# Kernel tuning notes

Hardware: AMD Instinct MI355X
Metric: run time of the kernel (lower is better)

The kernel has to match this reference:

```python
import jax, jax.numpy as jnp
import numpy as np

B, N, P, D, NH, DFFN = 4, 1024, 128, 512, 8, 2048
DH = D // NH  # 64


def setup_inputs() -> dict:
    key = jax.random.key(0)
    ks = jax.random.split(key, 64)
    i = [0]
    def rn(shape, s=1.0):
        k = ks[i[0]]; i[0] += 1
        return jax.random.normal(k, shape, jnp.float32) * s
    w = 0.05  # weight init scale
    inp = {
        "H": rn((B, N, D)),
        "V": rn((B, N, 3, D)),
        "D_batch": rn((B, N, N)),
        "rbf_bias": rn((B, 1, N, N)),  # rbf_feat_batch[layer_idx]
        "prompt_feature": rn((B * P, D)),
        # self-attn params
        "Wq": rn((4 * D, D), w), "bq": jnp.zeros((4 * D,), jnp.float32),
        "Wk": rn((4 * D, D), w), "bk": jnp.zeros((4 * D,), jnp.float32),
        "Wv": rn((D, D), w), "bv": jnp.zeros((D,), jnp.float32),
        "Wvv": rn((D, D), w),
        "Wo": rn((D, D), w), "bo": jnp.zeros((D,), jnp.float32),
        "Wvo": rn((D, D), w),
        "ln1_g": jnp.ones((D,), jnp.float32), "ln1_b": jnp.zeros((D,), jnp.float32),
        # cross-attn params (nn.MultiheadAttention packed in_proj + out_proj, then scaler_o)
        "ca_in_w": rn((3 * D, D), w), "ca_in_b": jnp.zeros((3 * D,), jnp.float32),
        "ca_out_w": rn((D, D), w), "ca_out_b": jnp.zeros((D,), jnp.float32),
        "ca_so_w": rn((D, D), w), "ca_so_b": jnp.zeros((D,), jnp.float32),
        "ln2_g": jnp.ones((D,), jnp.float32), "ln2_b": jnp.zeros((D,), jnp.float32),
        # GVP-FFN params
        "ffn_lv": rn((2 * D, D), w),
        "ffn_w1": rn((DFFN, 2 * D), w), "ffn_b1": jnp.zeros((DFFN,), jnp.float32),
        "ffn_w2": rn((2 * D, DFFN), w), "ffn_b2": jnp.zeros((2 * D,), jnp.float32),
        "ln3_g": jnp.ones((D,), jnp.float32), "ln3_b": jnp.zeros((D,), jnp.float32),
        # key-validity mask [B,N]
        "H_mask": jax.random.randint(ks[60], (B, N), 0, 2).astype(jnp.int32),
    }
    return inp


def _ln(x, g, b):
    m = x.mean(-1, keepdims=True)
    v = ((x - m) ** 2).mean(-1, keepdims=True)
    return (x - m) / jnp.sqrt(v + 1e-5) * g + b


def _ept_layer(H, V, D_batch, rbf_bias, prompt_feature,
               Wq, bq, Wk, bk, Wv, bv, Wvv, Wo, bo, Wvo, ln1_g, ln1_b,
               ca_in_w, ca_in_b, ca_out_w, ca_out_b, ca_so_w, ca_so_b, ln2_g, ln2_b,
               ffn_lv, ffn_w1, ffn_b1, ffn_w2, ffn_b2, ln3_g, ln3_b, H_mask):
    factor = 0.5 / np.sqrt(DH)
    # ---- self-attn sublayer (pre-LN on H, residual on H and V) ----
    H0, V0 = H, V
    Hn = _ln(H, ln1_g, ln1_b)
    Hq = (Hn @ Wq.T + bq).reshape(B, N, NH, 4 * DH)
    Hk = (Hn @ Wk.T + bk).reshape(B, N, NH, 4 * DH)
    Hv = (Hn @ Wv.T + bv).reshape(B, N, NH, DH)
    # vector values: [B,N,3,D] -> [B,N,3,NH,DH] -> [B,N,NH,3,DH] -> [B,N,NH,3*DH]
    Vv = (V @ Wvv.T).reshape(B, N, 3, NH, DH).transpose(0, 1, 3, 2, 4).reshape(B, N, NH, 3 * DH)
    V_attn = jnp.concatenate([Hv, Vv], axis=-1)  # [B,N,NH,4*DH]
    bias = rbf_bias + D_batch[:, None]           # [B,1,N,N]
    bias = jnp.where(H_mask[:, None, None, :] == 0, -jnp.inf, bias)
    scores = jnp.einsum('bnhd,bmhd->bhnm', Hq, Hk) * factor + bias
    attn = jax.nn.softmax(scores, axis=-1)
    res = jnp.einsum('bhnm,bmhd->bnhd', attn, V_attn)  # [B,N,NH,4*DH]
    H_res = res[..., :DH].reshape(B, N, D)
    V_res = res[..., DH:].reshape(B, N, NH, 3, DH).transpose(0, 1, 3, 2, 4).reshape(B, N, 3, D)
    H = (H_res @ Wo.T + bo) + H0
    V = (V_res @ Wvo.T) + V0
    # ---- cross-attn sublayer (pre-LN, residual on H only) ----
    H0 = H
    Hn = _ln(H, ln2_g, ln2_b)
    prompt = prompt_feature.reshape(B, P, D)
    Wq_c, Wk_c, Wv_c = ca_in_w[:D], ca_in_w[D:2 * D], ca_in_w[2 * D:]
    bq_c, bk_c, bv_c = ca_in_b[:D], ca_in_b[D:2 * D], ca_in_b[2 * D:]
    q = (Hn @ Wq_c.T + bq_c).reshape(B, N, NH, DH)
    k = (prompt @ Wk_c.T + bk_c).reshape(B, P, NH, DH)
    v = (prompt @ Wv_c.T + bv_c).reshape(B, P, NH, DH)
    ca = jax.nn.softmax(jnp.einsum('bnhd,bphd->bhnp', q, k) / np.sqrt(DH), axis=-1)
    co = jnp.einsum('bhnp,bphd->bnhd', ca, v).reshape(B, N, D)
    co = co @ ca_out_w.T + ca_out_b
    H = (co @ ca_so_w.T + ca_so_b) + H0
    # ---- GVP-FFN sublayer (pre-LN on H, residual on H and V) ----
    H0, V0 = H, V
    Hn = _ln(H, ln3_g, ln3_b)
    Vp = V @ ffn_lv.T                  # [B,N,3,2D]
    V1, V2 = Vp[..., :D], Vp[..., D:]
    scaler = jnp.concatenate([Hn, jnp.linalg.norm(V1, axis=-2)], axis=-1)  # [B,N,2D]
    h1 = jax.nn.silu(scaler @ ffn_w1.T + ffn_b1)
    so = h1 @ ffn_w2.T + ffn_b2        # [B,N,2D]
    H_out, V_upd = so[..., :D], so[..., D:]
    H = H_out + H0
    V = V_upd[..., None, :] * V2 + V0  # vector_act == 'none'
    return H, V


def reference(H, V, D_batch, rbf_bias, prompt_feature,
              Wq, bq, Wk, bk, Wv, bv, Wvv, Wo, bo, Wvo, ln1_g, ln1_b,
              ca_in_w, ca_in_b, ca_out_w, ca_out_b, ca_so_w, ca_so_b, ln2_g, ln2_b,
              ffn_lv, ffn_w1, ffn_b1, ffn_w2, ffn_b2, ln3_g, ln3_b, H_mask):
    return _ept_layer(H, V, D_batch, rbf_bias, prompt_feature,
                      Wq, bq, Wk, bk, Wv, bv, Wvv, Wo, bo, Wvo, ln1_g, ln1_b,
                      ca_in_w, ca_in_b, ca_out_w, ca_out_b, ca_so_w, ca_so_b, ln2_g, ln2_b,
                      ffn_lv, ffn_w1, ffn_b1, ffn_w2, ffn_b2, ln3_g, ln3_b, H_mask)
```

## Files before the change

### kernel.cpp

```cpp
#include <hip/hip_runtime.h>
#include <cstdint>
#include <cstddef>

#define B_    4
#define N_    1024
#define P_    128
#define D_    512
#define NH_   8
#define QKVW  4608

typedef unsigned short ushort_t;
typedef short short8 __attribute__((ext_vector_type(8)));
typedef float f32x4 __attribute__((ext_vector_type(4)));
typedef ushort_t ushort4_t __attribute__((ext_vector_type(4)));

__device__ inline ushort_t f2bf(float f) {
  union { float fp; unsigned int u; } v; v.fp = f;
  unsigned int r = v.u + 0x7fffu + ((v.u >> 16) & 1u);
  return (ushort_t)(r >> 16);
}
__device__ inline float bf2f(ushort_t u) {
  union { unsigned int i; float f; } v; v.i = ((unsigned int)u) << 16;
  return v.f;
}

__device__ __forceinline__ void gll16(const ushort_t* g, ushort_t* l) {
  __builtin_amdgcn_global_load_lds(
      (const __attribute__((address_space(1))) void*)g,
      (__attribute__((address_space(3))) void*)l, 16, 0, 0);
}

__device__ inline void cast8(const float* __restrict__ s, ushort_t* __restrict__ d,
                             unsigned i) {
  const float* sp = s + (size_t)i * 8;
  short8 o;
#pragma unroll
  for (int j = 0; j < 8; ++j) o[j] = (short)f2bf(sp[j]);
  *(short8*)(d + (size_t)i * 8) = o;
}

__global__ __launch_bounds__(256) void cast_fused(
    const float* s0, ushort_t* d0,  const float* s1, ushort_t* d1,
    const float* s2, ushort_t* d2,  const float* s3, ushort_t* d3,
    const float* s4, ushort_t* d4,  const float* s5, ushort_t* d5,
    const float* s6, ushort_t* d6,  const float* s7, ushort_t* d7,
    const float* s8, ushort_t* d8,  const float* s9, ushort_t* d9,
    const float* s10, ushort_t* d10, const float* s11, ushort_t* d11,
    const float* s12, ushort_t* d12, const float* s13, ushort_t* d13)
{
  unsigned i = blockIdx.x * 256 + threadIdx.x;
#define SEG(s, d, n8) if (i < (n8)) { cast8(s, d, i); return; } i -= (n8);
  SEG(s0, d0, 131072u)
  SEG(s1, d1, 131072u)
  SEG(s2, d2, 32768u)
  SEG(s3, d3, 32768u)
  SEG(s4, d4, 32768u)
  SEG(s5, d5, 32768u)
  SEG(s6, d6, 98304u)
  SEG(s7, d7, 32768u)
  SEG(s8, d8, 32768u)
  SEG(s9, d9, 65536u)
  SEG(s10, d10, 262144u)
  SEG(s11, d11, 262144u)
  SEG(s12, d12, 32768u)
  SEG(s13, d13, 786432u)
#undef SEG
}

__global__ __launch_bounds__(256) void biasmerge3(
    const float* __restrict__ bq, const float* __restrict__ bk,
    const float* __restrict__ bv, float* __restrict__ o)
{
  int i = blockIdx.x * 256 + threadIdx.x;
  if (i >= 4608) return;
  o[i] = (i < 2048) ? bq[i] : (i < 4096) ? bk[i - 2048] : bv[i - 4096];
}

__global__ __launch_bounds__(256) void biascomb(const float* __restrict__ Db,
                                                const float* __restrict__ rbf,
                                                const int* __restrict__ mask,
                                                ushort_t* __restrict__ out)
{
  size_t i = (size_t)blockIdx.x * 256 + threadIdx.x;
  size_t e = i * 4;
  int b  = (int)(e >> 20);
  int m0 = (int)(e & 1023);
  float4 r = *(const float4*)(rbf + e);
  float4 d = *(const float4*)(Db + e);
  const int* mp = mask + b * 1024 + m0;
  ushort4_t o;
  o.x = f2bf(mp[0] ? r.x + d.x : -1e30f);
  o.y = f2bf(mp[1] ? r.y + d.y : -1e30f);
  o.z = f2bf(mp[2] ? r.z + d.z : -1e30f);
  o.w = f2bf(mp[3] ? r.w + d.w : -1e30f);
  *(ushort4_t*)(out + e) = o;
}

__global__ __launch_bounds__(256) void ln_kernel(
    const float* __restrict__ x, const float* __restrict__ g,
    const float* __restrict__ bb, ushort_t* __restrict__ y, int ostride)
{
  int row = blockIdx.x;
  int t = threadIdx.x;
  const float* xr = x + (size_t)row * D_;
  float a = xr[t], c = xr[t + 256];
  float s = a + c, sq = a * a + c * c;
#pragma unroll
  for (int off = 32; off >= 1; off >>= 1) {
    s  += __shfl_xor(s, off);
    sq += __shfl_xor(sq, off);
  }
  __shared__ float red[8];
  int w = t >> 6, lane = t & 63;
  if (lane == 0) { red[w] = s; red[4 + w] = sq; }
  __syncthreads();
  float st  = red[0] + red[1] + red[2] + red[3];
  float sqt = red[4] + red[5] + red[6] + red[7];
  float mean = st * (1.0f / D_);
  float var  = sqt * (1.0f / D_) - mean * mean;
  float inv  = rsqrtf(var + 1e-5f);
  y[(size_t)row * ostride + t]       = f2bf((a - mean) * inv * g[t] + bb[t]);
  y[(size_t)row * ostride + t + 256] = f2bf((c - mean) * inv * g[t + 256] + bb[t + 256]);
}

__global__ __launch_bounds__(256) void gemm_bf16(
    const ushort_t* __restrict__ A, const ushort_t* __restrict__ W,
    const float* __restrict__ bias, const float* __restrict__ res,
    float* __restrict__ Cf, ushort_t* __restrict__ Cb,
    int M, int N, int K, int flags)
{
  __shared__ __align__(16) ushort_t Al[128 * 32];
  __shared__ __align__(16) ushort_t Wl[128 * 32];
  const int t = threadIdx.x;
  const int wv = t >> 6, lane = t & 63, lr = lane & 15, lk = lane >> 4;
  const int wr = wv >> 1, wc = wv & 1;

  const int gx = gridDim.x;
  const int lid = blockIdx.y * gx + blockIdx.x;
  const int cpx = (gx * gridDim.y) >> 3;
  const int nlid = (lid & 7) * cpx + (lid >> 3);
  const size_t row0 = (size_t)(nlid / gx) * 128;
  const size_t col0 = (size_t)(nlid % gx) * 128;

  const int srow = 32 * wv + (lane >> 2);
  const int scol = (((lane & 3) ^ ((lane >> 3) & 3))) * 8;
  const ushort_t* ApG = A + (row0 + srow) * (size_t)K + scol;
  const ushort_t* WpG = W + (col0 + srow) * (size_t)K + scol;
  ushort_t* AlD = Al + (size_t)(32 * wv) * 32;
  ushort_t* WlD = Wl + (size_t)(32 * wv) * 32;
  const size_t K16 = (size_t)16 * K;

  f32x4 acc[4][4];
#pragma unroll
  for (int i = 0; i < 4; ++i)
#pragma unroll
    for (int j = 0; j < 4; ++j) acc[i][j] = f32x4{0.f, 0.f, 0.f, 0.f};

  const int sx = (lr >> 1) & 3;

  for (int k0 = 0; k0 < K; k0 += 32) {
    __syncthreads();
    gll16(ApG + k0,       AlD);
    gll16(ApG + k0 + K16, AlD + 512);
    gll16(WpG + k0,       WlD);
    gll16(WpG + k0 + K16, WlD + 512);
    __syncthreads();
    short8 af[4], bf[4];
#pragma unroll
    for (int i = 0; i < 4; ++i)
      af[i] = *(const short8*)&Al[(wr * 64 + i * 16 + lr) * 32 + ((lk ^ sx) << 3)];
#pragma unroll
    for (int j = 0; j < 4; ++j)
      bf[j] = *(const short8*)&Wl[(wc * 64 + j * 16 + lr) * 32 + ((lk ^ sx) << 3)];
#pragma unroll
    for (int i = 0; i < 4; ++i)
#pragma unroll
      for (int j = 0; j < 4; ++j)
        acc[i][j] = __builtin_amdgcn_mfma_f32_16x16x32_bf16(af[i], bf[j], acc[i][j], 0, 0, 0);
  }

  const int orow = wr * 64 + lk * 4, ocol = wc * 64 + lr;
#pragma unroll
  for (int i = 0; i < 4; ++i) {
#pragma unroll
    for (int j = 0; j < 4; ++j) {
      size_t colb = col0 + ocol + j * 16;
      float bv = (flags & 1) ? bias[colb] : 0.f;
#pragma unroll
      for (int r = 0; r < 4; ++r) {
        size_t rowg = row0 + orow + i * 16 + r;
        float v = acc[i][j][r] + bv;
        if (flags & 4) v = v / (1.f + __expf(-v));
        if (flags & 2) v += res[rowg * N + colb];
        if (flags & 8)  Cf[rowg * N + colb] = v;
        if (flags & 16) Cb[rowg * N + colb] = f2bf(v);
      }
    }
  }
}

__global__ __launch_bounds__(256) void gemm_bf16_sm(
    const ushort_t* __restrict__ A, const ushort_t* __restrict__ W,
    const float* __restrict__ bias, const float* __restrict__ res,
    float* __restrict__ Cf, ushort_t* __restrict__ Cb,
    int M, int N, int K, int flags)
{
  __shared__ __align__(16) ushort_t Al[64 * 32];
  __shared__ __align__(16) ushort_t Wl[128 * 32];
  const int t = threadIdx.x;
  const int wv = t >> 6, lane = t & 63, lr = lane & 15, lk = lane >> 4;
  const int wr = wv >> 1, wc = wv & 1;

  const int gx = gridDim.x;
  const int lid = blockIdx.y * gx + blockIdx.x;
  const int cpx = (gx * gridDim.y) >> 3;
  const int nlid = (lid & 7) * cpx + (lid >> 3);
  const size_t row0 = (size_t)(nlid / gx) * 64;
  const size_t col0 = (size_t)(nlid % gx) * 128;

  const int scol = (((lane & 3) ^ ((lane >> 3) & 3))) * 8;
  const int srowA = 16 * wv + (lane >> 2);
  const int srowW = 32 * wv + (lane >> 2);
  const ushort_t* ApG = A + (row0 + srowA) * (size_t)K + scol;
  const ushort_t* WpG = W + (col0 + srowW) * (size_t)K + scol;
  ushort_t* AlD = Al + (size_t)(16 * wv) * 32;
  ushort_t* WlD = Wl + (size_t)(32 * wv) * 32;
  const size_t K16 = (size_t)16 * K;

  f32x4 acc[2][4];
#pragma unroll
  for (int i = 0; i < 2; ++i)
#pragma unroll
    for (int j = 0; j < 4; ++j) acc[i][j] = f32x4{0.f, 0.f, 0.f, 0.f};

  const int sx = (lr >> 1) & 3;

  for (int k0 = 0; k0 < K; k0 += 32) {
    __syncthreads();
    gll16(ApG + k0,       AlD);
    gll16(WpG + k0,       WlD);
    gll16(WpG + k0 + K16, WlD + 512);
    __syncthreads();
    short8 af[2], bf[4];
#pragma unroll
    for (int i = 0; i < 2; ++i)
      af[i] = *(const short8*)&Al[(wr * 32 + i * 16 + lr) * 32 + ((lk ^ sx) << 3)];
#pragma unroll
    for (int j = 0; j < 4; ++j)
      bf[j] = *(const short8*)&Wl[(wc * 64 + j * 16 + lr) * 32 + ((lk ^ sx) << 3)];
#pragma unroll
    for (int i = 0; i < 2; ++i)
#pragma unroll
      for (int j = 0; j < 4; ++j)
        acc[i][j] = __builtin_amdgcn_mfma_f32_16x16x32_bf16(af[i], bf[j], acc[i][j], 0, 0, 0);
  }

  const int orow = wr * 32 + lk * 4, ocol = wc * 64 + lr;
#pragma unroll
  for (int i = 0; i < 2; ++i) {
#pragma unroll
    for (int j = 0; j < 4; ++j) {
      size_t colb = col0 + ocol + j * 16;
      float bv = (flags & 1) ? bias[colb] : 0.f;
#pragma unroll
      for (int r = 0; r < 4; ++r) {
        size_t rowg = row0 + orow + i * 16 + r;
        float v = acc[i][j][r] + bv;
        if (flags & 4) v = v / (1.f + __expf(-v));
        if (flags & 2) v += res[rowg * N + colb];
        if (flags & 8)  Cf[rowg * N + colb] = v;
        if (flags & 16) Cb[rowg * N + colb] = f2bf(v);
      }
    }
  }
}

__global__ __launch_bounds__(256) void vt_build(
    const ushort_t* __restrict__ QKVb, const ushort_t* __restrict__ VVTb,
    ushort_t* __restrict__ VT)
{
  const int bh = blockIdx.z, b = bh >> 3, h = bh & 7;
  const int n0 = blockIdx.x * 64, dt = blockIdx.y;
  __shared__ __align__(16) ushort_t tile[64][72];
  const int t = threadIdx.x;
  {
    int r = t >> 2, c0 = (t & 3) * 16;
    const ushort_t* src = (dt == 0)
      ? QKVb + ((size_t)(b * 1024 + n0 + r)) * QKVW + 4096 + h * 64 + c0
      : VVTb + (((size_t)(b * 1024 + n0 + r)) * 3 + (dt - 1)) * 512 + h * 64 + c0;
    *(short8*)&tile[r][c0]     = *(const short8*)src;
    *(short8*)&tile[r][c0 + 8] = *(const short8*)(src + 8);
  }
  __syncthreads();
  {
    int d = t >> 2, nc = (t & 3) * 16;
    short8 o0, o1;
#pragma unroll
    for (int i = 0; i < 8; ++i) { o0[i] = tile[nc + i][d]; o1[i] = tile[nc + 8 + i][d]; }
    ushort_t* dst = VT + ((size_t)bh * 256 + dt * 64 + d) * 1024 + n0 + nc;
    *(short8*)dst = o0;
    *(short8*)(dst + 8) = o1;
  }
}

__global__ __launch_bounds__(256) void attn_mfma(
    const ushort_t* __restrict__ QKg, const ushort_t* __restrict__ VTg,
    const ushort_t* __restrict__ biasb,
    ushort_t* __restrict__ HRESb, ushort_t* __restrict__ VRESb)
{
  const int blk = blockIdx.x;
  const int bi = blk >> 3;
  const int bh = (blk & 7) * 4 + (bi >> 4), b = bh >> 3, h = bh & 7;
  const int q0 = (bi & 15) * 64;
  const int t = threadIdx.x, w = t >> 6, lane = t & 63, lr = lane & 15, lk = lane >> 4;

  __shared__ __align__(16) ushort_t Kl[32][268];
  __shared__ __align__(16) ushort_t Vl[256][40];
  __shared__ __align__(16) ushort_t Pl[4][16][40];

  short8 qf[8];
  {
    const ushort_t* qb = QKg + ((size_t)(b * 1024 + q0 + w * 16 + lr)) * QKVW + h * 256;
#pragma unroll
    for (int s = 0; s < 8; ++s) qf[s] = *(const short8*)(qb + s * 32 + lk * 8);
  }
  f32x4 o[16];
#pragma unroll
  for (int i = 0; i < 16; ++i) o[i] = f32x4{0.f, 0.f, 0.f, 0.f};
  float mrow[4] = {-1e30f, -1e30f, -1e30f, -1e30f};
  float lsum[4] = {0.f, 0.f, 0.f, 0.f};
  const int qrow = q0 + w * 16 + lk * 4;

  const int krow = t >> 3, kc = (t & 7) * 32;
  const ushort_t* ksrc = QKg + ((size_t)(b * 1024 + krow)) * QKVW + 2048 + h * 256 + kc;
  const ushort_t* vsrc = VTg + ((size_t)bh * 256 + t) * 1024;
  const int vrot = (t >> 3) & 3;

  for (int k0 = 0; k0 < 1024; k0 += 32) {
    __syncthreads();
    {
      const ushort_t* ks = ksrc + (size_t)k0 * QKVW;
#pragma unroll
      for (int c = 0; c < 4; ++c)
        *(short8*)&Kl[krow][kc + c * 8] = *(const short8*)(ks + c * 8);
#pragma unroll
      for (int c = 0; c < 4; ++c) {
        int cc = (c + vrot) & 3;
        *(short8*)&Vl[t][cc * 8] = *(const short8*)(vsrc + k0 + cc * 8);
      }
    }
    __syncthreads();

    f32x4 s2[2];
    s2[0] = f32x4{0.f, 0.f, 0.f, 0.f};
    s2[1] = f32x4{0.f, 0.f, 0.f, 0.f};
    __builtin_amdgcn_s_setprio(1);
#pragma unroll
    for (int ks = 0; ks < 8; ++ks) {
#pragma unroll
      for (int j = 0; j < 2; ++j) {
        short8 kf = *(const short8*)&Kl[j * 16 + lr][ks * 32 + lk * 8];
        s2[j] = __builtin_amdgcn_mfma_f32_16x16x32_bf16(qf[ks], kf, s2[j], 0, 0, 0);
      }
    }
    __builtin_amdgcn_s_setprio(0);

    float sv[2][4];
    const ushort_t* bp = biasb + ((size_t)b << 20) + (size_t)qrow * 1024 + k0 + lr;
#pragma unroll
    for (int r = 0; r < 4; ++r) {
      sv[0][r] = s2[0][r] * 0.0625f + bf2f(bp[r * 1024]);
      sv[1][r] = s2[1][r] * 0.0625f + bf2f(bp[r * 1024 + 16]);
    }
    float pm[4], need = -1e30f;
#pragma unroll
    for (int r = 0; r < 4; ++r) {
      float m2 = fmaxf(sv[0][r], sv[1][r]);
      m2 = fmaxf(m2, __shfl_xor(m2, 1));
      m2 = fmaxf(m2, __shfl_xor(m2, 2));
      m2 = fmaxf(m2, __shfl_xor(m2, 4));
      m2 = fmaxf(m2, __shfl_xor(m2, 8));
      pm[r] = m2;
      need = fmaxf(need, m2 - mrow[r]);
    }
    if (!__all(need <= 8.f)) {
#pragma unroll
      for (int r = 0; r < 4; ++r) {
        float mn = fmaxf(mrow[r], pm[r]);
        float al = __expf(mrow[r] - mn);
        mrow[r] = mn;
        lsum[r] *= al;
#pragma unroll
        for (int d = 0; d < 16; ++d) o[d][r] *= al;
      }
    }
#pragma unroll
    for (int r = 0; r < 4; ++r) {
      float p0 = __expf(sv[0][r] - mrow[r]);
      float p1 = __expf(sv[1][r] - mrow[r]);
      float rs = p0 + p1;
      rs += __shfl_xor(rs, 1); rs += __shfl_xor(rs, 2);
      rs += __shfl_xor(rs, 4); rs += __shfl_xor(rs, 8);
      lsum[r] += rs;
      Pl[w][lk * 4 + r][lr]      = f2bf(p0);
      Pl[w][lk * 4 + r][16 + lr] = f2bf(p1);
    }
    short8 pf = *(const short8*)&Pl[w][lr][lk * 8];
    __builtin_amdgcn_s_setprio(1);
#pragma unroll
    for (int d = 0; d < 16; ++d) {
      short8 vf = *(const short8*)&Vl[d * 16 + lr][lk * 8];
      o[d] = __builtin_amdgcn_mfma_f32_16x16x32_bf16(pf, vf, o[d], 0, 0, 0);
    }
    __builtin_amdgcn_s_setprio(0);
  }

  float inv[4];
#pragma unroll
  for (int r = 0; r < 4; ++r) inv[r] = 1.f / lsum[r];
#pragma unroll
  for (int d = 0; d < 16; ++d) {
    int dcat = d * 16 + lr;
#pragma unroll
    for (int r = 0; r < 4; ++r) {
      float v = o[d][r] * inv[r];
      int n = qrow + r;
      if (dcat < 64)
        HRESb[((size_t)b * 1024 + n) * 512 + h * 64 + dcat] = f2bf(v);
      else {
        int c = (dcat - 64) >> 6, jj = (dcat - 64) & 63;
        VRESb[(((size_t)b * 1024 + n) * 3 + c) * 512 + h * 64 + jj] = f2bf(v);
      }
    }
  }
}

__global__ __launch_bounds__(256) void attn_cross_mfma(
    const ushort_t* __restrict__ Qb, const ushort_t* __restrict__ KVb,
    ushort_t* __restrict__ COb)
{
  const int bh = blockIdx.y, b = bh >> 3, h = bh & 7;
  const int q0 = blockIdx.x * 64;
  const int t = threadIdx.x, w = t >> 6, lane = t & 63, lr = lane & 15, lk = lane >> 4;

  __shared__ __align__(16) ushort_t Kl[128][72];
  __shared__ __align__(16) ushort_t Vt[64][136];
  __shared__ __align__(16) ushort_t Pl[4][16][136];

  {
    int p = t >> 1, c0 = (t & 1) * 32;
    const ushort_t* kp = KVb + ((size_t)b * 128 + p) * 1024 + h * 64 + c0;
#pragma unroll
    for (int i = 0; i < 4; ++i) {
      short8 kv = *(const short8*)(kp + i * 8);
      *(short8*)&Kl[p][c0 + i * 8] = kv;
      short8 vv = *(const short8*)(kp + 512 + i * 8);
#pragma unroll
      for (int jj = 0; jj < 8; ++jj) Vt[c0 + i * 8 + jj][p] = (ushort_t)vv[jj];
    }
  }
  __syncthreads();

  short8 qf[2];
  {
    const ushort_t* qp = Qb + ((size_t)b * 1024 + q0 + w * 16 + lr) * 512 + h * 64;
    qf[0] = *(const short8*)(qp + lk * 8);
    qf[1] = *(const short8*)(qp + 32 + lk * 8);
  }

  f32x4 s[8];
#pragma unroll
  for (int j = 0; j < 8; ++j) s[j] = f32x4{0.f, 0.f, 0.f, 0.f};
#pragma unroll
  for (int ks = 0; ks < 2; ++ks)
#pragma unroll
    for (int j = 0; j < 8; ++j) {
      short8 kf = *(const short8*)&Kl[j * 16 + lr][ks * 32 + lk * 8];
      s[j] = __builtin_amdgcn_mfma_f32_16x16x32_bf16(qf[ks], kf, s[j], 0, 0, 0);
    }

  float linv[4];
#pragma unroll
  for (int r = 0; r < 4; ++r) {
    float sc[8];
#pragma unroll
    for (int j = 0; j < 8; ++j) sc[j] = s[j][r] * 0.125f;
    float mx = sc[0];
#pragma unroll
    for (int j = 1; j < 8; ++j) mx = fmaxf(mx, sc[j]);
    mx = fmaxf(mx, __shfl_xor(mx, 1));
    mx = fmaxf(mx, __shfl_xor(mx, 2));
    mx = fmaxf(mx, __shfl_xor(mx, 4));
    mx = fmaxf(mx, __shfl_xor(mx, 8));
    float rs = 0.f;
#pragma unroll
    for (int j = 0; j < 8; ++j) {
      float p = __expf(sc[j] - mx);
      rs += p;
      Pl[w][lk * 4 + r][j * 16 + lr] = f2bf(p);
    }
    rs += __shfl_xor(rs, 1); rs += __shfl_xor(rs, 2);
    rs += __shfl_xor(rs, 4); rs += __shfl_xor(rs, 8);
    linv[r] = 1.f / rs;
  }
  __syncthreads();

  f32x4 o[4];
#pragma unroll
  for (int d = 0; d < 4; ++d) o[d] = f32x4{0.f, 0.f, 0.f, 0.f};
#pragma unroll
  for (int ks = 0; ks < 4; ++ks) {
    short8 pf = *(const short8*)&Pl[w][lr][ks * 32 + lk * 8];
#pragma unroll
    for (int d = 0; d < 4; ++d) {
      short8 vf = *(const short8*)&Vt[d * 16 + lr][ks * 32 + lk * 8];
      o[d] = __builtin_amdgcn_mfma_f32_16x16x32_bf16(pf, vf, o[d], 0, 0, 0);
    }
  }

#pragma unroll
  for (int d = 0; d < 4; ++d)
#pragma unroll
    for (int r = 0; r < 4; ++r) {
      int n = q0 + w * 16 + lk * 4 + r;
      COb[((size_t)b * 1024 + n) * 512 + h * 64 + d * 16 + lr] = f2bf(o[d][r] * linv[r]);
    }
}

__global__ __launch_bounds__(256) void vnorm_kernel(
    const ushort_t* __restrict__ Vp, ushort_t* __restrict__ scal)
{
  size_t i = (size_t)blockIdx.x * 256 + threadIdx.x;
  size_t bn = i >> 9; int d = (int)(i & 511);
  size_t base = bn * 3 * 1024 + d;
  float a = bf2f(Vp[base]);
  float b = bf2f(Vp[base + 1024]);
  float c = bf2f(Vp[base + 2048]);
  scal[bn * 1024 + 512 + d] = f2bf(sqrtf(a * a + b * b + c * c));
}

__global__ __launch_bounds__(256) void final_kernel(
    const float* __restrict__ so, const float* __restrict__ H2,
    const ushort_t* __restrict__ Vp, const float* __restrict__ Vnew,
    float* __restrict__ out)
{
  size_t i = (size_t)blockIdx.x * 256 + threadIdx.x;
  size_t bn = i >> 9; int d = (int)(i & 511);
  out[bn * 512 + d] = so[bn * 1024 + d] + H2[bn * 512 + d];
  float vu = so[bn * 1024 + 512 + d];
  float* outV = out + (size_t)B_ * N_ * D_;
#pragma unroll
  for (int c = 0; c < 3; ++c) {
    size_t vi = (bn * 3 + c) * 512 + d;
    outV[vi] = vu * bf2f(Vp[(bn * 3 + c) * 1024 + 512 + d]) + Vnew[vi];
  }
}

extern "C" void kernel_launch(void* const* d_in, const int* in_sizes, int n_in,
                              void* d_out, int out_size, void* d_ws, size_t ws_size,
                              hipStream_t stream)
{
  const float* H      = (const float*)d_in[0];
  const float* V      = (const float*)d_in[1];
  const float* Db     = (const float*)d_in[2];
  const float* rbf    = (const float*)d_in[3];
  const float* prompt = (const float*)d_in[4];
  const float* Wq  = (const float*)d_in[5];
  const float* bq  = (const float*)d_in[6];
  const float* Wk  = (const float*)d_in[7];
  const float* bk  = (const float*)d_in[8];
  const float* Wv  = (const float*)d_in[9];
  const float* bv  = (const float*)d_in[10];
  const float* Wvv = (const float*)d_in[11];
  const float* Wo  = (const float*)d_in[12];
  const float* bo  = (const float*)d_in[13];
  const float* Wvo = (const float*)d_in[14];
  const float* ln1g = (const float*)d_in[15];
  const float* ln1b = (const float*)d_in[16];
  const float* caw  = (const float*)d_in[17];
  const float* cab  = (const float*)d_in[18];
  const float* caow = (const float*)d_in[19];
  const float* caob = (const float*)d_in[20];
  const float* casw = (const float*)d_in[21];
  const float* casb = (const float*)d_in[22];
  const float* ln2g = (const float*)d_in[23];
  const float* ln2b = (const float*)d_in[24];
  const float* flv  = (const float*)d_in[25];
  const float* fw1  = (const float*)d_in[26];
  const float* fb1  = (const float*)d_in[27];
  const float* fw2  = (const float*)d_in[28];
  const float* fb2  = (const float*)d_in[29];
  const float* ln3g = (const float*)d_in[30];
  const float* ln3b = (const float*)d_in[31];
  const int*   mask = (const int*)d_in[32];

  char* wsb = (char*)d_ws;
  float* out = (float*)d_out;

#define HMB(x) ((size_t)(x) << 19)
  ushort_t* Wqkvb = (ushort_t*)(wsb + HMB(0));
  ushort_t* Wvvb  = (ushort_t*)(wsb + HMB(9));
  ushort_t* Wob   = (ushort_t*)(wsb + HMB(10));
  ushort_t* Wvob  = (ushort_t*)(wsb + HMB(11));
  ushort_t* cawb  = (ushort_t*)(wsb + HMB(12));
  ushort_t* caowb = (ushort_t*)(wsb + HMB(15));
  ushort_t* caswb = (ushort_t*)(wsb + HMB(16));
  ushort_t* flvb  = (ushort_t*)(wsb + HMB(17));
  ushort_t* fw1b  = (ushort_t*)(wsb + HMB(19));
  ushort_t* fw2b  = (ushort_t*)(wsb + HMB(27));
  ushort_t* promptb = (ushort_t*)(wsb + HMB(35));
  float*    BQKV  = (float*)   (wsb + HMB(36));
  ushort_t* HQKVb = (ushort_t*)(wsb + HMB(37));
  float*    VNEW  = (float*)   (wsb + HMB(37));
  ushort_t* VNEWb = (ushort_t*)(wsb + HMB(85));
  float*    SO    = (float*)   (wsb + HMB(85));
  ushort_t* VVTb  = (ushort_t*)(wsb + HMB(109));
  ushort_t* HN2b  = (ushort_t*)(wsb + HMB(109));
  ushort_t* QCb   = (ushort_t*)(wsb + HMB(117));
  ushort_t* KVCb  = (ushort_t*)(wsb + HMB(125));
  ushort_t* COb   = (ushort_t*)(wsb + HMB(127));
  ushort_t* Vb    = (ushort_t*)(wsb + HMB(133));
  ushort_t* HRESb = (ushort_t*)(wsb + HMB(133));
  ushort_t* CO2b  = (ushort_t*)(wsb + HMB(135));
  ushort_t* VRESb = (ushort_t*)(wsb + HMB(141));
  float*    H2    = (float*)   (wsb + HMB(143));
  ushort_t* HNb   = (ushort_t*)(wsb + HMB(157));
  ushort_t* VPb   = (ushort_t*)(wsb + HMB(159));
  ushort_t* VT    = (ushort_t*)(wsb + HMB(165));
  ushort_t* BIASCb= (ushort_t*)(wsb + HMB(197));
  float*    H1    = (float*)   (wsb + HMB(213));
  ushort_t* SCALb = (ushort_t*)(wsb + HMB(207));
  ushort_t* HH1b  = (ushort_t*)(wsb + HMB(223));

  cast_fused<<<7680, 256, 0, stream>>>(
      Wq, Wqkvb, Wk, Wqkvb + (size_t)2048 * 512, Wv, Wqkvb + (size_t)4096 * 512,
      Wvv, Wvvb, Wo, Wob, Wvo, Wvob, caw, cawb, caow, caowb, casw, caswb,
      flv, flvb, fw1, fw1b, fw2, fw2b, prompt, promptb, V, Vb);
  biasmerge3<<<18, 256, 0, stream>>>(bq, bk, bv, BQKV);
  biascomb<<<4096, 256, 0, stream>>>(Db, rbf, mask, BIASCb);
  ln_kernel<<<4096, 256, 0, stream>>>(H, ln1g, ln1b, HNb, 512);

  gemm_bf16<<<dim3(36, 32), 256, 0, stream>>>(HNb, Wqkvb, BQKV, nullptr, nullptr, HQKVb, 4096, 4608, 512, 1 | 16);
  gemm_bf16<<<dim3(4, 96), 256, 0, stream>>>(Vb, Wvvb, nullptr, nullptr, nullptr, VVTb, 12288, 512, 512, 16);

  vt_build<<<dim3(16, 4, 32), 256, 0, stream>>>(HQKVb, VVTb, VT);

  attn_mfma<<<512, 256, 0, stream>>>(HQKVb, VT, BIASCb, HRESb, VRESb);

  gemm_bf16_sm<<<dim3(4, 64), 256, 0, stream>>>(HRESb, Wob, bo, H, H1, nullptr, 4096, 512, 512, 1 | 2 | 8);
  gemm_bf16<<<dim3(4, 96), 256, 0, stream>>>(VRESb, Wvob, nullptr, V, VNEW, VNEWb, 12288, 512, 512, 2 | 8 | 16);

  ln_kernel<<<4096, 256, 0, stream>>>(H1, ln2g, ln2b, HN2b, 512);
  gemm_bf16_sm<<<dim3(4, 64), 256, 0, stream>>>(HN2b, cawb, cab, nullptr, nullptr, QCb, 4096, 512, 512, 1 | 16);
  gemm_bf16_sm<<<dim3(8, 8), 256, 0, stream>>>(promptb, cawb + 262144, cab + 512, nullptr, nullptr, KVCb, 512, 1024, 512, 1 | 16);

  attn_cross_mfma<<<dim3(16, 32), 256, 0, stream>>>(QCb, KVCb, COb);

  gemm_bf16_sm<<<dim3(4, 64), 256, 0, stream>>>(COb, caowb, caob, nullptr, nullptr, CO2b, 4096, 512, 512, 1 | 16);
  gemm_bf16_sm<<<dim3(4, 64), 256, 0, stream>>>(CO2b, caswb, casb, H1, H2, nullptr, 4096, 512, 512, 1 | 2 | 8);

  gemm_bf16<<<dim3(8, 96), 256, 0, stream>>>(VNEWb, flvb, nullptr, nullptr, nullptr, VPb, 12288, 1024, 512, 16);
  ln_kernel<<<4096, 256, 0, stream>>>(H2, ln3g, ln3b, SCALb, 1024);
  vnorm_kernel<<<8192, 256, 0, stream>>>(VPb, SCALb);

  gemm_bf16<<<dim3(16, 32), 256, 0, stream>>>(SCALb, fw1b, fb1, nullptr, nullptr, HH1b, 4096, 2048, 1024, 1 | 4 | 16);
  gemm_bf16_sm<<<dim3(8, 64), 256, 0, stream>>>(HH1b, fw2b, fb2, nullptr, SO, nullptr, 4096, 1024, 2048, 1 | 8);

  final_kernel<<<8192, 256, 0, stream>>>(SO, H2, VPb, VNEW, out);

  (void)in_sizes; (void)n_in; (void)out_size; (void)ws_size;
}
```

Before: 467.6 us.

## Fuse prologue kernels into one launch and final residual into FFN2 epilogue

```diff
diff --git a/kernel.cpp b/kernel.cpp
--- a/kernel.cpp
+++ b/kernel.cpp
@@ -39,61 +39,85 @@
   *(short8*)(d + (size_t)i * 8) = o;
 }
 
-__global__ __launch_bounds__(256) void cast_fused(
+__global__ __launch_bounds__(256) void p0_fused(
     const float* s0, ushort_t* d0,  const float* s1, ushort_t* d1,
     const float* s2, ushort_t* d2,  const float* s3, ushort_t* d3,
     const float* s4, ushort_t* d4,  const float* s5, ushort_t* d5,
     const float* s6, ushort_t* d6,  const float* s7, ushort_t* d7,
     const float* s8, ushort_t* d8,  const float* s9, ushort_t* d9,
     const float* s10, ushort_t* d10, const float* s11, ushort_t* d11,
-    const float* s12, ushort_t* d12, const float* s13, ushort_t* d13)
-{
-  unsigned i = blockIdx.x * 256 + threadIdx.x;
+    const float* s12, ushort_t* d12, const float* s13, ushort_t* d13,
+    const float* bq, const float* bk, const float* bv, float* bqkv,
+    const float* Db, const float* rbf, const int* mask, ushort_t* biasc,
+    const float* Hx, const float* g1, const float* b1, ushort_t* hn)
+{
+  const int blk = blockIdx.x;
+  const int tid = threadIdx.x;
+
+  if (blk < 7680) {
+    unsigned i = blk * 256 + tid;
 #define SEG(s, d, n8) if (i < (n8)) { cast8(s, d, i); return; } i -= (n8);
-  SEG(s0, d0, 131072u)
-  SEG(s1, d1, 131072u)
-  SEG(s2, d2, 32768u)
-  SEG(s3, d3, 32768u)
-  SEG(s4, d4, 32768u)
-  SEG(s5, d5, 32768u)
-  SEG(s6, d6, 98304u)
-  SEG(s7, d7, 32768u)
-  SEG(s8, d8, 32768u)
-  SEG(s9, d9, 65536u)
-  SEG(s10, d10, 262144u)
-  SEG(s11, d11, 262144u)
-  SEG(s12, d12, 32768u)
-  SEG(s13, d13, 786432u)
+    SEG(s0, d0, 131072u)
+    SEG(s1, d1, 131072u)
+    SEG(s2, d2, 32768u)
+    SEG(s3, d3, 32768u)
+    SEG(s4, d4, 32768u)
+    SEG(s5, d5, 32768u)
+    SEG(s6, d6, 98304u)
+    SEG(s7, d7, 32768u)
+    SEG(s8, d8, 32768u)
+    SEG(s9, d9, 65536u)
+    SEG(s10, d10, 262144u)
+    SEG(s11, d11, 262144u)
+    SEG(s12, d12, 32768u)
+    SEG(s13, d13, 786432u)
 #undef SEG
-}
-
-__global__ __launch_bounds__(256) void biasmerge3(
-    const float* __restrict__ bq, const float* __restrict__ bk,
-    const float* __restrict__ bv, float* __restrict__ o)
-{
-  int i = blockIdx.x * 256 + threadIdx.x;
-  if (i >= 4608) return;
-  o[i] = (i < 2048) ? bq[i] : (i < 4096) ? bk[i - 2048] : bv[i - 4096];
-}
-
-__global__ __launch_bounds__(256) void biascomb(const float* __restrict__ Db,
-                                                const float* __restrict__ rbf,
-                                                const int* __restrict__ mask,
-                                                ushort_t* __restrict__ out)
-{
-  size_t i = (size_t)blockIdx.x * 256 + threadIdx.x;
-  size_t e = i * 4;
-  int b  = (int)(e >> 20);
-  int m0 = (int)(e & 1023);
-  float4 r = *(const float4*)(rbf + e);
-  float4 d = *(const float4*)(Db + e);
-  const int* mp = mask + b * 1024 + m0;
-  ushort4_t o;
-  o.x = f2bf(mp[0] ? r.x + d.x : -1e30f);
-  o.y = f2bf(mp[1] ? r.y + d.y : -1e30f);
-  o.z = f2bf(mp[2] ? r.z + d.z : -1e30f);
-  o.w = f2bf(mp[3] ? r.w + d.w : -1e30f);
-  *(ushort4_t*)(out + e) = o;
+    return;
+  }
+  if (blk < 7698) {
+    int i = (blk - 7680) * 256 + tid;
+    if (i < 4608)
+      bqkv[i] = (i < 2048) ? bq[i] : (i < 4096) ? bk[i - 2048] : bv[i - 4096];
+    return;
+  }
+  if (blk < 11794) {
+    size_t i = (size_t)(blk - 7698) * 256 + tid;
+    size_t e = i * 4;
+    int b  = (int)(e >> 20);
+    int m0 = (int)(e & 1023);
+    float4 r = *(const float4*)(rbf + e);
+    float4 d = *(const float4*)(Db + e);
+    const int* mp = mask + b * 1024 + m0;
+    ushort4_t o;
+    o.x = f2bf(mp[0] ? r.x + d.x : -1e30f);
+    o.y = f2bf(mp[1] ? r.y + d.y : -1e30f);
+    o.z = f2bf(mp[2] ? r.z + d.z : -1e30f);
+    o.w = f2bf(mp[3] ? r.w + d.w : -1e30f);
+    *(ushort4_t*)(biasc + e) = o;
+    return;
+  }
+  {
+    int row = blk - 11794;
+    const float* xr = Hx + (size_t)row * D_;
+    float a = xr[tid], c = xr[tid + 256];
+    float s = a + c, sq = a * a + c * c;
+#pragma unroll
+    for (int off = 32; off >= 1; off >>= 1) {
+      s  += __shfl_xor(s, off);
+      sq += __shfl_xor(sq, off);
+    }
+    __shared__ float red[8];
+    int w = tid >> 6, lane = tid & 63;
+    if (lane == 0) { red[w] = s; red[4 + w] = sq; }
+    __syncthreads();
+    float st  = red[0] + red[1] + red[2] + red[3];
+    float sqt = red[4] + red[5] + red[6] + red[7];
+    float mean = st * (1.0f / D_);
+    float var  = sqt * (1.0f / D_) - mean * mean;
+    float inv  = rsqrtf(var + 1e-5f);
+    hn[(size_t)row * 512 + tid]       = f2bf((a - mean) * inv * g1[tid] + b1[tid]);
+    hn[(size_t)row * 512 + tid + 256] = f2bf((c - mean) * inv * g1[tid + 256] + b1[tid + 256]);
+  }
 }
 
 __global__ __launch_bounds__(256) void ln_kernel(
@@ -203,6 +227,7 @@
     const ushort_t* __restrict__ A, const ushort_t* __restrict__ W,
     const float* __restrict__ bias, const float* __restrict__ res,
     float* __restrict__ Cf, ushort_t* __restrict__ Cb,
+    const ushort_t* __restrict__ Vp, const float* __restrict__ Vnw,
     int M, int N, int K, int flags)
 {
   __shared__ __align__(16) ushort_t Al[64 * 32];
@@ -267,6 +292,20 @@
         size_t rowg = row0 + orow + i * 16 + r;
         float v = acc[i][j][r] + bv;
         if (flags & 4) v = v / (1.f + __expf(-v));
+        if (flags & 32) {
+          if (colb < 512) {
+            Cf[rowg * 512 + colb] = v + res[rowg * 512 + colb];
+          } else {
+            int dd = (int)colb - 512;
+            float* outV = Cf + (size_t)4096 * 512;
+#pragma unroll
+            for (int c = 0; c < 3; ++c) {
+              size_t vi = (rowg * 3 + c) * 512 + dd;
+              outV[vi] = v * bf2f(Vp[(rowg * 3 + c) * 1024 + 512 + dd]) + Vnw[vi];
+            }
+          }
+          continue;
+        }
         if (flags & 2) v += res[rowg * N + colb];
         if (flags & 8)  Cf[rowg * N + colb] = v;
         if (flags & 16) Cb[rowg * N + colb] = f2bf(v);
@@ -537,23 +576,6 @@
   float b = bf2f(Vp[base + 1024]);
   float c = bf2f(Vp[base + 2048]);
   scal[bn * 1024 + 512 + d] = f2bf(sqrtf(a * a + b * b + c * c));
-}
-
-__global__ __launch_bounds__(256) void final_kernel(
-    const float* __restrict__ so, const float* __restrict__ H2,
-    const ushort_t* __restrict__ Vp, const float* __restrict__ Vnew,
-    float* __restrict__ out)
-{
-  size_t i = (size_t)blockIdx.x * 256 + threadIdx.x;
-  size_t bn = i >> 9; int d = (int)(i & 511);
-  out[bn * 512 + d] = so[bn * 1024 + d] + H2[bn * 512 + d];
-  float vu = so[bn * 1024 + 512 + d];
-  float* outV = out + (size_t)B_ * N_ * D_;
-#pragma unroll
-  for (int c = 0; c < 3; ++c) {
-    size_t vi = (bn * 3 + c) * 512 + d;
-    outV[vi] = vu * bf2f(Vp[(bn * 3 + c) * 1024 + 512 + d]) + Vnew[vi];
-  }
 }
 
 extern "C" void kernel_launch(void* const* d_in, const int* in_sizes, int n_in,
@@ -613,7 +635,6 @@
   ushort_t* HQKVb = (ushort_t*)(wsb + HMB(37));
   float*    VNEW  = (float*)   (wsb + HMB(37));
   ushort_t* VNEWb = (ushort_t*)(wsb + HMB(85));
-  float*    SO    = (float*)   (wsb + HMB(85));
   ushort_t* VVTb  = (ushort_t*)(wsb + HMB(109));
   ushort_t* HN2b  = (ushort_t*)(wsb + HMB(109));
   ushort_t* QCb   = (ushort_t*)(wsb + HMB(117));
@@ -632,13 +653,11 @@
   ushort_t* SCALb = (ushort_t*)(wsb + HMB(207));
   ushort_t* HH1b  = (ushort_t*)(wsb + HMB(223));
 
-  cast_fused<<<7680, 256, 0, stream>>>(
+  p0_fused<<<15890, 256, 0, stream>>>(
       Wq, Wqkvb, Wk, Wqkvb + (size_t)2048 * 512, Wv, Wqkvb + (size_t)4096 * 512,
       Wvv, Wvvb, Wo, Wob, Wvo, Wvob, caw, cawb, caow, caowb, casw, caswb,
-      flv, flvb, fw1, fw1b, fw2, fw2b, prompt, promptb, V, Vb);
-  biasmerge3<<<18, 256, 0, stream>>>(bq, bk, bv, BQKV);
-  biascomb<<<4096, 256, 0, stream>>>(Db, rbf, mask, BIASCb);
-  ln_kernel<<<4096, 256, 0, stream>>>(H, ln1g, ln1b, HNb, 512);
+      flv, flvb, fw1, fw1b, fw2, fw2b, prompt, promptb, V, Vb,
+      bq, bk, bv, BQKV, Db, rbf, mask, BIASCb, H, ln1g, ln1b, HNb);
 
   gemm_bf16<<<dim3(36, 32), 256, 0, stream>>>(HNb, Wqkvb, BQKV, nullptr, nullptr, HQKVb, 4096, 4608, 512, 1 | 16);
   gemm_bf16<<<dim3(4, 96), 256, 0, stream>>>(Vb, Wvvb, nullptr, nullptr, nullptr, VVTb, 12288, 512, 512, 16);
@@ -647,26 +666,24 @@
 
   attn_mfma<<<512, 256, 0, stream>>>(HQKVb, VT, BIASCb, HRESb, VRESb);
 
-  gemm_bf16_sm<<<dim3(4, 64), 256, 0, stream>>>(HRESb, Wob, bo, H, H1, nullptr, 4096, 512, 512, 1 | 2 | 8);
+  gemm_bf16_sm<<<dim3(4, 64), 256, 0, stream>>>(HRESb, Wob, bo, H, H1, nullptr, nullptr, nullptr, 4096, 512, 512, 1 | 2 | 8);
   gemm_bf16<<<dim3(4, 96), 256, 0, stream>>>(VRESb, Wvob, nullptr, V, VNEW, VNEWb, 12288, 512, 512, 2 | 8 | 16);
 
   ln_kernel<<<4096, 256, 0, stream>>>(H1, ln2g, ln2b, HN2b, 512);
-  gemm_bf16_sm<<<dim3(4, 64), 256, 0, stream>>>(HN2b, cawb, cab, nullptr, nullptr, QCb, 4096, 512, 512, 1 | 16);
-  gemm_bf16_sm<<<dim3(8, 8), 256, 0, stream>>>(promptb, cawb + 262144, cab + 512, nullptr, nullptr, KVCb, 512, 1024, 512, 1 | 16);
+  gemm_bf16_sm<<<dim3(4, 64), 256, 0, stream>>>(HN2b, cawb, cab, nullptr, nullptr, QCb, nullptr, nullptr, 4096, 512, 512, 1 | 16);
+  gemm_bf16_sm<<<dim3(8, 8), 256, 0, stream>>>(promptb, cawb + 262144, cab + 512, nullptr, nullptr, KVCb, nullptr, nullptr, 512, 1024, 512, 1 | 16);
 
   attn_cross_mfma<<<dim3(16, 32), 256, 0, stream>>>(QCb, KVCb, COb);
 
-  gemm_bf16_sm<<<dim3(4, 64), 256, 0, stream>>>(COb, caowb, caob, nullptr, nullptr, CO2b, 4096, 512, 512, 1 | 16);
-  gemm_bf16_sm<<<dim3(4, 64), 256, 0, stream>>>(CO2b, caswb, casb, H1, H2, nullptr, 4096, 512, 512, 1 | 2 | 8);
+  gemm_bf16_sm<<<dim3(4, 64), 256, 0, stream>>>(COb, caowb, caob, nullptr, nullptr, CO2b, nullptr, nullptr, 4096, 512, 512, 1 | 16);
+  gemm_bf16_sm<<<dim3(4, 64), 256, 0, stream>>>(CO2b, caswb, casb, H1, H2, nullptr, nullptr, nullptr, 4096, 512, 512, 1 | 2 | 8);
 
   gemm_bf16<<<dim3(8, 96), 256, 0, stream>>>(VNEWb, flvb, nullptr, nullptr, nullptr, VPb, 12288, 1024, 512, 16);
   ln_kernel<<<4096, 256, 0, stream>>>(H2, ln3g, ln3b, SCALb, 1024);
   vnorm_kernel<<<8192, 256, 0, stream>>>(VPb, SCALb);
 
   gemm_bf16<<<dim3(16, 32), 256, 0, stream>>>(SCALb, fw1b, fb1, nullptr, nullptr, HH1b, 4096, 2048, 1024, 1 | 4 | 16);
-  gemm_bf16_sm<<<dim3(8, 64), 256, 0, stream>>>(HH1b, fw2b, fb2, nullptr, SO, nullptr, 4096, 1024, 2048, 1 | 8);
-
-  final_kernel<<<8192, 256, 0, stream>>>(SO, H2, VPb, VNEW, out);
+  gemm_bf16_sm<<<dim3(8, 64), 256, 0, stream>>>(HH1b, fw2b, fb2, H2, out, nullptr, VPb, VNEW, 4096, 1024, 2048, 1 | 32);
 
   (void)in_sizes; (void)n_in; (void)out_size; (void)ws_size;
 }
```

Result: no change. 460.0 us (-1.6%).
